# Optimization experiments

Measured on AMD Instinct MI355X. Metric: run time of the kernel, lower is better.

Reference implementation:

```python
import jax, jax.numpy as jnp
import numpy as np

N_HEAD = 4
N_FEAT = 256
D_K = N_FEAT // N_HEAD


def setup_inputs() -> dict:
    key = jax.random.key(0)
    ks = jax.random.split(key, 7)
    B, T, F = 8, 2048, N_FEAT
    return {
        "query": jax.random.normal(ks[0], (B, T, F), dtype=jnp.float32),
        "key": jax.random.normal(ks[1], (B, T, F), dtype=jnp.float32),
        "value": jax.random.normal(ks[2], (B, T, F), dtype=jnp.float32),
        "mask": jax.random.randint(ks[3], (B, 1, T), 0, 2, dtype=jnp.int32),
        "W_qkv": jax.random.normal(ks[4], (3 * F, 3 * F), dtype=jnp.float32) * 0.02,
        "b_qkv": jnp.zeros((3 * F,), dtype=jnp.float32),
        "W_out": jax.random.normal(ks[5], (F, F), dtype=jnp.float32) * 0.02,
        "b_out": jnp.zeros((F,), dtype=jnp.float32),
    }


def reference(query, key, value, mask, W_qkv, b_qkv, W_out, b_out):
    B, T, F = query.shape
    H, dk = N_HEAD, D_K
    # fused QKV projection on concatenated [q; k; v]  -> (B, T, 3F)
    qkv = jnp.concatenate([query, key, value], axis=-1) @ W_qkv.T + b_qkv
    qkv = qkv.reshape(B, T, H, 3 * dk)
    q, k, v = jnp.split(qkv, 3, axis=-1)          # each (B, T, H, dk)
    q = q.transpose(0, 2, 1, 3)                    # (B, H, T, dk)
    k = k.transpose(0, 2, 1, 3)
    v = v.transpose(0, 2, 1, 3)
    scores = jnp.einsum("bhqd,bhkd->bhqk", q, k) / jnp.sqrt(jnp.float32(dk))
    # mask: (B, 1, T) -> broadcast (B, 1, 1, T); positions where mask==0 are masked
    m = (mask[:, None, :, :] == 0)
    min_val = jnp.finfo(scores.dtype).min
    scores = jnp.where(m, min_val, scores)
    attn = jax.nn.softmax(scores, axis=-1)
    attn = jnp.where(m, jnp.float32(0.0), attn)    # zero masked probs, as in torch code
    x = jnp.einsum("bhqk,bhkd->bhqd", attn, v)     # (B, H, T, dk)
    x = x.transpose(0, 2, 1, 3).reshape(B, T, H * dk)
    return x @ W_out.T + b_out
```

## Files before the change

### kernel.cpp

```cpp
#include <hip/hip_runtime.h>
#include <hip/hip_bf16.h>

#define NB 8
#define NT 2048
#define NH 4
#define NF 256
#define NTF 768
#define NM (NB * NT)

typedef unsigned short u16;
typedef unsigned int u32;
typedef unsigned long long u64;
typedef u16 u16x8 __attribute__((ext_vector_type(8)));
typedef __bf16 bf16x8 __attribute__((ext_vector_type(8)));
typedef float f32x4 __attribute__((ext_vector_type(4)));
typedef float f32x16 __attribute__((ext_vector_type(16)));

__device__ __forceinline__ u16 bf16_rne(float f) {
    union { float f; unsigned u; } x; x.f = f;
    unsigned u = x.u;
    return (u16)((u + 0x7fffu + ((u >> 16) & 1u)) >> 16);
}

__device__ __forceinline__ int swz(int row, int colB) {
    return row * 128 + (colB ^ ((row & 7) << 4));
}

__device__ __forceinline__ void glds16(const void* g, void* l) {
    __builtin_amdgcn_global_load_lds(
        (const __attribute__((address_space(1))) void*)g,
        (__attribute__((address_space(3))) void*)l, 16, 0, 0);
}

__device__ __forceinline__ u32 pkbf16(float lo, float hi) {
    union { __bf16 h2[2]; u32 u; } t;
    t.h2[0] = (__bf16)lo; t.h2[1] = (__bf16)hi;
    return t.u;
}

__device__ __forceinline__ void pl32swap(u32& a, u32& b) {
    asm("v_permlane32_swap_b32 %0, %1" : "+v"(a), "+v"(b));
}

#define mfma16(A, B, C) __builtin_amdgcn_mfma_f32_16x16x32_bf16((A), (B), (C), 0, 0, 0)
#define mfma32(A, B, C) __builtin_amdgcn_mfma_f32_32x32x16_bf16((A), (B), (C), 0, 0, 0)

__global__ __launch_bounds__(256) void convert_all_kernel(
        const float* __restrict__ q, const float* __restrict__ k,
        const float* __restrict__ v, const float* __restrict__ wqkv,
        const float* __restrict__ wout, const int* __restrict__ mask,
        u16* __restrict__ xcat, u16* __restrict__ wqkvb,
        u16* __restrict__ woutb, float* __restrict__ maskadd) {
    int bid = blockIdx.x;
    if (bid < 6144) {
        int tid = bid * 256 + threadIdx.x;
        int row = tid / 96;
        int c8  = (tid % 96) * 8;
        const float* src; int c;
        if (c8 < NF)            { src = q; c = c8; }
        else if (c8 < 2 * NF)   { src = k; c = c8 - NF; }
        else                    { src = v; c = c8 - 2 * NF; }
        const float4* p = reinterpret_cast<const float4*>(src + (size_t)row * NF + c);
        float4 a = p[0], b = p[1];
        u16x8 o;
        o[0] = bf16_rne(a.x); o[1] = bf16_rne(a.y); o[2] = bf16_rne(a.z); o[3] = bf16_rne(a.w);
        o[4] = bf16_rne(b.x); o[5] = bf16_rne(b.y); o[6] = bf16_rne(b.z); o[7] = bf16_rne(b.w);
        *reinterpret_cast<u16x8*>(xcat + (size_t)row * NTF + c8) = o;
    } else if (bid < 6464) {
        int tid = (bid - 6144) * 256 + threadIdx.x;
        int i8 = tid * 8;
        const float* src; u16* dst; int off;
        if (i8 < NTF * NTF) { src = wqkv; dst = wqkvb; off = i8; }
        else                { src = wout; dst = woutb; off = i8 - NTF * NTF; }
        const float4* p = reinterpret_cast<const float4*>(src + off);
        float4 a = p[0], b = p[1];
        u16x8 o;
        o[0] = bf16_rne(a.x); o[1] = bf16_rne(a.y); o[2] = bf16_rne(a.z); o[3] = bf16_rne(a.w);
        o[4] = bf16_rne(b.x); o[5] = bf16_rne(b.y); o[6] = bf16_rne(b.z); o[7] = bf16_rne(b.w);
        *reinterpret_cast<u16x8*>(dst + off) = o;
    } else {
        int i = (bid - 6464) * 2048 + threadIdx.x * 8;
        int4 m0 = *reinterpret_cast<const int4*>(mask + i);
        int4 m1 = *reinterpret_cast<const int4*>(mask + i + 4);
        float4 f0 = { m0.x ? 0.f : -1e30f, m0.y ? 0.f : -1e30f,
                      m0.z ? 0.f : -1e30f, m0.w ? 0.f : -1e30f };
        float4 f1 = { m1.x ? 0.f : -1e30f, m1.y ? 0.f : -1e30f,
                      m1.z ? 0.f : -1e30f, m1.w ? 0.f : -1e30f };
        *reinterpret_cast<float4*>(maskadd + i) = f0;
        *reinterpret_cast<float4*>(maskadd + i + 4) = f1;
    }
}

__global__ __launch_bounds__(256) void gemm128_qkv_kernel(
        const u16* __restrict__ A, const u16* __restrict__ Bw,
        const float* __restrict__ bias, u16* __restrict__ QKV,
        u16* __restrict__ Vt) {
    __shared__ alignas(16) char smem[65536];
    char* As = smem;
    char* Bs = smem + 32768;
    constexpr int K = NTF;
    int m0 = blockIdx.x * 128, n0 = blockIdx.y * 128;
    int tid = threadIdx.x;
    int w = tid >> 6, lane = tid & 63, l15 = lane & 15, hi = lane >> 4;
    int wr = w >> 1, wc = w & 1;
    int r0 = tid >> 3, cb0 = (tid & 7) * 16;
    int gcb = cb0 ^ ((r0 & 7) << 4);
    int wo = w * 1024;

    const char* Ac = (const char*)A;
    const char* Bc = (const char*)Bw;
    const char* gA = Ac + (size_t)(m0 + r0) * (K * 2) + gcb;
    const char* gB = Bc + (size_t)(n0 + r0) * (K * 2) + gcb;
    const size_t rstep = (size_t)32 * (K * 2);

#pragma unroll
    for (int p = 0; p < 4; ++p) {
        glds16(gA + p * rstep, As + p * 4096 + wo);
        glds16(gB + p * rstep, Bs + p * 4096 + wo);
    }

    f32x4 acc[4][4];
#pragma unroll
    for (int fi = 0; fi < 4; ++fi)
#pragma unroll
        for (int fj = 0; fj < 4; ++fj) acc[fi][fj] = (f32x4){0.f, 0.f, 0.f, 0.f};

    constexpr int NKT = K / 64;
    for (int kt = 0; kt < NKT; ++kt) {
        int cur = kt & 1;
        __syncthreads();
        if (kt + 1 < NKT) {
            int off = (kt + 1) * 128;
            char* Ad = As + (cur ^ 1) * 16384;
            char* Bd = Bs + (cur ^ 1) * 16384;
#pragma unroll
            for (int p = 0; p < 4; ++p) {
                glds16(gA + p * rstep + off, Ad + p * 4096 + wo);
                glds16(gB + p * rstep + off, Bd + p * 4096 + wo);
            }
        }
        const char* Ax = As + cur * 16384;
        const char* Bx = Bs + cur * 16384;
#pragma unroll
        for (int ks = 0; ks < 2; ++ks) {
            bf16x8 af[4], bf[4];
#pragma unroll
            for (int fi = 0; fi < 4; ++fi)
                af[fi] = *reinterpret_cast<const bf16x8*>(
                    Ax + swz(wr * 64 + fi * 16 + l15, hi * 16 + ks * 64));
#pragma unroll
            for (int fj = 0; fj < 4; ++fj)
                bf[fj] = *reinterpret_cast<const bf16x8*>(
                    Bx + swz(wc * 64 + fj * 16 + l15, hi * 16 + ks * 64));
#pragma unroll
            for (int fi = 0; fi < 4; ++fi)
#pragma unroll
                for (int fj = 0; fj < 4; ++fj)
                    acc[fi][fj] = mfma16(af[fi], bf[fj], acc[fi][fj]);
        }
    }

    int g64 = (n0 >> 6) + wc;
    int typ = g64 % 3, h = g64 / 3;
    int rowBase = m0 + wr * 64;
    if (typ == 2) {
        int b = rowBase >> 11;
        int bh = b * NH + h;
#pragma unroll
        for (int fi = 0; fi < 4; ++fi) {
            int t = (rowBase + fi * 16 + hi * 4) & (NT - 1);
#pragma unroll
            for (int fj = 0; fj < 4; ++fj) {
                int d = fj * 16 + l15;
                float bv = bias[n0 + wc * 64 + d];
                u32 lo = pkbf16(acc[fi][fj][0] + bv, acc[fi][fj][1] + bv);
                u32 hi2 = pkbf16(acc[fi][fj][2] + bv, acc[fi][fj][3] + bv);
                u64 pk = (u64)lo | ((u64)hi2 << 32);
                *reinterpret_cast<u64*>(Vt + (size_t)(bh * 64 + d) * NT + t) = pk;
            }
        }
    } else {
#pragma unroll
        for (int fi = 0; fi < 4; ++fi) {
            int orow = rowBase + fi * 16 + hi * 4;
#pragma unroll
            for (int fj = 0; fj < 4; ++fj) {
                int col = n0 + wc * 64 + fj * 16 + l15;
                float bv = bias[col];
#pragma unroll
                for (int r = 0; r < 4; ++r)
                    QKV[(size_t)(orow + r) * NTF + col] = bf16_rne(acc[fi][fj][r] + bv);
            }
        }
    }
}

template<int N, int K>
__global__ __launch_bounds__(256) void gemm_kernel(
        const u16* __restrict__ A, const u16* __restrict__ Bw,
        const float* __restrict__ bias, float* __restrict__ Cout) {
    __shared__ alignas(16) char smem[32768];
    char* As = smem;
    char* Bs = smem + 16384;
    int m0 = blockIdx.x * 64, n0 = blockIdx.y * 64;
    int tid = threadIdx.x;
    int w = tid >> 6, lane = tid & 63, l15 = lane & 15, hi = lane >> 4;
    int r0 = tid >> 3, cb0 = (tid & 7) * 16;
    int gcb = cb0 ^ ((r0 & 7) << 4);
    int wo = w * 1024;

    const char* Ac = (const char*)A;
    const char* Bc = (const char*)Bw;
    const char* ga0 = Ac + (size_t)(m0 + r0) * (K * 2) + gcb;
    const char* ga1 = ga0 + (size_t)32 * (K * 2);
    const char* gb0 = Bc + (size_t)(n0 + r0) * (K * 2) + gcb;
    const char* gb1 = gb0 + (size_t)32 * (K * 2);

    glds16(ga0, As + wo); glds16(ga1, As + 4096 + wo);
    glds16(gb0, Bs + wo); glds16(gb1, Bs + 4096 + wo);

    f32x4 acc[4];
#pragma unroll
    for (int ct = 0; ct < 4; ++ct) acc[ct] = (f32x4){0.f, 0.f, 0.f, 0.f};

    constexpr int NKT = K / 64;
    for (int kt = 0; kt < NKT; ++kt) {
        int cur = kt & 1;
        __syncthreads();
        if (kt + 1 < NKT) {
            int off = (kt + 1) * 128;
            char* Ad = As + (cur ^ 1) * 8192;
            char* Bd = Bs + (cur ^ 1) * 8192;
            glds16(ga0 + off, Ad + wo); glds16(ga1 + off, Ad + 4096 + wo);
            glds16(gb0 + off, Bd + wo); glds16(gb1 + off, Bd + 4096 + wo);
        }
        const char* Ax = As + cur * 8192;
        const char* Bx = Bs + cur * 8192;
#pragma unroll
        for (int ks = 0; ks < 2; ++ks) {
            bf16x8 af = *reinterpret_cast<const bf16x8*>(Ax + swz(w * 16 + l15, hi * 16 + ks * 64));
#pragma unroll
            for (int ct = 0; ct < 4; ++ct) {
                bf16x8 bf = *reinterpret_cast<const bf16x8*>(Bx + swz(ct * 16 + l15, hi * 16 + ks * 64));
                acc[ct] = mfma16(af, bf, acc[ct]);
            }
        }
    }

    int orow = m0 + w * 16 + hi * 4;
#pragma unroll
    for (int ct = 0; ct < 4; ++ct) {
        int col = n0 + ct * 16 + l15;
        float bv = bias[col];
#pragma unroll
        for (int r = 0; r < 4; ++r)
            Cout[(size_t)(orow + r) * N + col] = acc[ct][r] + bv;
    }
}

__global__ __launch_bounds__(512, 4) void attn_kernel(
        const u16* __restrict__ qkv, const u16* __restrict__ vt,
        const float* __restrict__ maskadd, u16* __restrict__ xout) {
    int bh = blockIdx.x;
    int q0 = blockIdx.y * 128;
    int b = bh >> 2, h = bh & 3;
    __shared__ alignas(16) char smem[65536];
    int tid = threadIdx.x;
    int w = tid >> 6, lane = tid & 63;
    int l31 = lane & 31, hv = lane >> 5;
    int wq = w & 3, g = w >> 2;
    int r0 = tid >> 3, cb0 = (tid & 7) * 16;
    int gcb = cb0 ^ ((r0 & 7) << 4);
    int wo = w * 1024;
    const float SCALE = 0.125f * 1.44269504088896340736f;

    const char* qkvC = (const char*)qkv;
    const char* vtC  = (const char*)vt;
    const char* gk0 = qkvC + (size_t)(b * NT + r0) * 1536 + h * 384 + 128 + gcb;
    const char* gv0 = vtC + (size_t)(bh * 64 + r0) * (NT * 2) + gcb;

    glds16(gk0,         smem + wo);
    glds16(gk0 + 98304, smem + 8192 + wo);
    glds16(gv0,         smem + 32768 + wo);
    glds16(gv0 + 128,   smem + 32768 + 8192 + wo);

    const char* qrow = qkvC + (size_t)(b * NT + q0 + wq * 32 + l31) * 1536
                       + h * 384 + hv * 16;
    bf16x8 bQ0 = *reinterpret_cast<const bf16x8*>(qrow);
    bf16x8 bQ1 = *reinterpret_cast<const bf16x8*>(qrow + 32);
    bf16x8 bQ2 = *reinterpret_cast<const bf16x8*>(qrow + 64);
    bf16x8 bQ3 = *reinterpret_cast<const bf16x8*>(qrow + 96);

    f32x16 accO0 = 0.f, accO1 = 0.f;
    float ssum = 0.f;
    const float* gm = maskadd + (size_t)b * NT;

    for (int j = 0; j < 16; ++j) {
        int cur = j & 1;
        __syncthreads();
        if (j < 15) {
            int tn = 2 * (j + 1);
            char* Kd = smem + (cur ^ 1) * 16384;
            char* Vd = smem + 32768 + (cur ^ 1) * 16384;
            glds16(gk0 + (size_t)tn * 98304, Kd + wo);
            glds16(gk0 + (size_t)(tn + 1) * 98304, Kd + 8192 + wo);
            glds16(gv0 + (size_t)tn * 128, Vd + wo);
            glds16(gv0 + (size_t)(tn + 1) * 128, Vd + 8192 + wo);
        }
        int t = 2 * j + g;
        const char* Kx = smem + g * 8192 + cur * 16384;
        const char* Vx = smem + 32768 + g * 8192 + cur * 16384;

        f32x16 s0 = 0.f, s1 = 0.f;
        __builtin_amdgcn_s_setprio(1);
#pragma unroll
        for (int ks = 0; ks < 4; ++ks) {
            bf16x8 a0 = *reinterpret_cast<const bf16x8*>(Kx + swz(l31, ks * 32 + hv * 16));
            bf16x8 a1 = *reinterpret_cast<const bf16x8*>(Kx + swz(32 + l31, ks * 32 + hv * 16));
            bf16x8 bq = (ks == 0) ? bQ0 : (ks == 1) ? bQ1 : (ks == 2) ? bQ2 : bQ3;
            s0 = mfma32(a0, bq, s0);
            s1 = mfma32(a1, bq, s1);
        }
        __builtin_amdgcn_s_setprio(0);

        const float* mt = gm + t * 64;
#pragma unroll
        for (int rq = 0; rq < 4; ++rq) {
            f32x4 md0 = *reinterpret_cast<const f32x4*>(mt + rq * 8 + 4 * hv);
            f32x4 md1 = *reinterpret_cast<const f32x4*>(mt + 32 + rq * 8 + 4 * hv);
#pragma unroll
            for (int e = 0; e < 4; ++e) {
                s0[rq * 4 + e] = __builtin_amdgcn_exp2f(
                    __builtin_fmaf(s0[rq * 4 + e], SCALE, md0[e]));
                s1[rq * 4 + e] = __builtin_amdgcn_exp2f(
                    __builtin_fmaf(s1[rq * 4 + e], SCALE, md1[e]));
            }
        }
        {
            f32x16 rv = s0 + s1;
            union { f32x16 v; f32x4 q[4]; } u; u.v = rv;
            f32x4 r4 = (u.q[0] + u.q[1]) + (u.q[2] + u.q[3]);
            ssum += (r4[0] + r4[1]) + (r4[2] + r4[3]);
        }

        u32 pka0[4], pkb0[4], pka1[4], pkb1[4];
#pragma unroll
        for (int rq = 0; rq < 4; ++rq) {
            pka0[rq] = pkbf16(s0[rq * 4 + 0], s0[rq * 4 + 1]);
            pkb0[rq] = pkbf16(s0[rq * 4 + 2], s0[rq * 4 + 3]);
            pka1[rq] = pkbf16(s1[rq * 4 + 0], s1[rq * 4 + 1]);
            pkb1[rq] = pkbf16(s1[rq * 4 + 2], s1[rq * 4 + 3]);
        }
        __builtin_amdgcn_s_setprio(1);
#pragma unroll
        for (int s4 = 0; s4 < 4; ++s4) {
            const int kb = s4 >> 1, sp = (s4 & 1) * 2;
            u32 B0, B1, B2, B3;
            if (kb == 0) { B0 = pka0[sp]; B2 = pka0[sp + 1]; B1 = pkb0[sp]; B3 = pkb0[sp + 1]; }
            else         { B0 = pka1[sp]; B2 = pka1[sp + 1]; B1 = pkb1[sp]; B3 = pkb1[sp + 1]; }
            pl32swap(B0, B2);
            pl32swap(B1, B3);
            union { u32 u4[4]; bf16x8 v; } bp;
            bp.u4[0] = B0; bp.u4[1] = B1; bp.u4[2] = B2; bp.u4[3] = B3;
            bf16x8 av0 = *reinterpret_cast<const bf16x8*>(Vx + swz(l31, s4 * 32 + hv * 16));
            bf16x8 av1 = *reinterpret_cast<const bf16x8*>(Vx + swz(32 + l31, s4 * 32 + hv * 16));
            accO0 = mfma32(av0, bp.v, accO0);
            accO1 = mfma32(av1, bp.v, accO1);
        }
        __builtin_amdgcn_s_setprio(0);
    }

    ssum += __shfl_xor(ssum, 32, 64);
    __syncthreads();
    float* sS = reinterpret_cast<float*>(smem + 32768);
    if (g == 1) {
        union { f32x16 v; f32x4 q[4]; } o0, o1; o0.v = accO0; o1.v = accO1;
#pragma unroll
        for (int i = 0; i < 4; ++i) {
            *reinterpret_cast<f32x4*>(smem + wq * 8192 + i * 1024 + lane * 16) = o0.q[i];
            *reinterpret_cast<f32x4*>(smem + wq * 8192 + (4 + i) * 1024 + lane * 16) = o1.q[i];
        }
        if (lane < 32) sS[wq * 32 + l31] = ssum;
    }
    __syncthreads();
    if (g == 0) {
        union { f32x16 v; f32x4 q[4]; } o0, o1; o0.v = accO0; o1.v = accO1;
#pragma unroll
        for (int i = 0; i < 4; ++i) {
            o0.q[i] += *reinterpret_cast<const f32x4*>(smem + wq * 8192 + i * 1024 + lane * 16);
            o1.q[i] += *reinterpret_cast<const f32x4*>(smem + wq * 8192 + (4 + i) * 1024 + lane * 16);
        }
        float stot = ssum + sS[wq * 32 + l31];
        float inv = stot > 0.f ? 1.0f / stot : 0.0f;
        int qg = b * NT + q0 + wq * 32 + l31;
#pragma unroll
        for (int db = 0; db < 2; ++db) {
            const float* of = db ? (const float*)&o1.v : (const float*)&o0.v;
#pragma unroll
            for (int rq = 0; rq < 4; ++rq) {
                u32 lo = pkbf16(of[rq * 4 + 0] * inv, of[rq * 4 + 1] * inv);
                u32 hi2 = pkbf16(of[rq * 4 + 2] * inv, of[rq * 4 + 3] * inv);
                u64 pk = (u64)lo | ((u64)hi2 << 32);
                int d = db * 32 + rq * 8 + 4 * hv;
                *reinterpret_cast<u64*>(xout + (size_t)qg * NF + h * 64 + d) = pk;
            }
        }
    }
}

extern "C" void kernel_launch(void* const* d_in, const int* in_sizes, int n_in,
                              void* d_out, int out_size, void* d_ws, size_t ws_size,
                              hipStream_t stream) {
    const float* q    = (const float*)d_in[0];
    const float* k    = (const float*)d_in[1];
    const float* v    = (const float*)d_in[2];
    const int*   mask = (const int*)d_in[3];
    const float* wqkv = (const float*)d_in[4];
    const float* bqkv = (const float*)d_in[5];
    const float* wout = (const float*)d_in[6];
    const float* bout = (const float*)d_in[7];
    float* out = (float*)d_out;

    char* ws = (char*)d_ws;
    u16*   Xcat    = (u16*)(ws);
    u16*   QKV     = (u16*)(ws + 25165824);
    u16*   Vt      = (u16*)(ws + 50331648);
    u16*   Xattn   = (u16*)(ws + 58720256);
    u16*   Wqkvb   = (u16*)(ws + 67108864);
    u16*   Woutb   = (u16*)(ws + 68288512);
    float* Maskadd = (float*)(ws + 68419584);

    convert_all_kernel<<<6472, 256, 0, stream>>>(q, k, v, wqkv, wout, mask,
                                                 Xcat, Wqkvb, Woutb, Maskadd);
    gemm128_qkv_kernel<<<dim3(NM / 128, NTF / 128), 256, 0, stream>>>(
        Xcat, Wqkvb, bqkv, QKV, Vt);
    attn_kernel<<<dim3(NB * NH, NT / 128), 512, 0, stream>>>(QKV, Vt, Maskadd, Xattn);
    gemm_kernel<NF, NF><<<dim3(NM / 64, NF / 64), 256, 0, stream>>>(
        Xattn, Woutb, bout, out);
}
```

Before: 101.2 us.

## Fuse fp32-to-bf16 activation conversion into QKV GEMM A-tile loading

Removes the separate conversion of query/key/value into a concatenated bf16 buffer. The QKV GEMM now loads fp32 activations directly into registers, converts them to bf16 and stores them into swizzled shared memory, with the load overlapped with the MFMA loop. This avoids writing and re-reading a 24 MB intermediate and one large kernel launch. In exchange, each A tile is read in fp32 by every column block and converted redundantly, which raises register use (launch bounds set to 2 blocks per CU).

After: 104.2 us. 3.0% more time.

```diff
diff --git a/kernel.cpp b/kernel.cpp
--- a/kernel.cpp
+++ b/kernel.cpp
@@ -12,6 +12,7 @@
 typedef unsigned int u32;
 typedef unsigned long long u64;
 typedef u16 u16x8 __attribute__((ext_vector_type(8)));
+typedef u32 u32x4 __attribute__((ext_vector_type(4)));
 typedef __bf16 bf16x8 __attribute__((ext_vector_type(8)));
 typedef float f32x4 __attribute__((ext_vector_type(4)));
 typedef float f32x16 __attribute__((ext_vector_type(16)));
@@ -45,29 +46,13 @@
 #define mfma16(A, B, C) __builtin_amdgcn_mfma_f32_16x16x32_bf16((A), (B), (C), 0, 0, 0)
 #define mfma32(A, B, C) __builtin_amdgcn_mfma_f32_32x32x16_bf16((A), (B), (C), 0, 0, 0)
 
-__global__ __launch_bounds__(256) void convert_all_kernel(
-        const float* __restrict__ q, const float* __restrict__ k,
-        const float* __restrict__ v, const float* __restrict__ wqkv,
-        const float* __restrict__ wout, const int* __restrict__ mask,
-        u16* __restrict__ xcat, u16* __restrict__ wqkvb,
+__global__ __launch_bounds__(256) void convert_wm_kernel(
+        const float* __restrict__ wqkv, const float* __restrict__ wout,
+        const int* __restrict__ mask, u16* __restrict__ wqkvb,
         u16* __restrict__ woutb, float* __restrict__ maskadd) {
     int bid = blockIdx.x;
-    if (bid < 6144) {
+    if (bid < 320) {
         int tid = bid * 256 + threadIdx.x;
-        int row = tid / 96;
-        int c8  = (tid % 96) * 8;
-        const float* src; int c;
-        if (c8 < NF)            { src = q; c = c8; }
-        else if (c8 < 2 * NF)   { src = k; c = c8 - NF; }
-        else                    { src = v; c = c8 - 2 * NF; }
-        const float4* p = reinterpret_cast<const float4*>(src + (size_t)row * NF + c);
-        float4 a = p[0], b = p[1];
-        u16x8 o;
-        o[0] = bf16_rne(a.x); o[1] = bf16_rne(a.y); o[2] = bf16_rne(a.z); o[3] = bf16_rne(a.w);
-        o[4] = bf16_rne(b.x); o[5] = bf16_rne(b.y); o[6] = bf16_rne(b.z); o[7] = bf16_rne(b.w);
-        *reinterpret_cast<u16x8*>(xcat + (size_t)row * NTF + c8) = o;
-    } else if (bid < 6464) {
-        int tid = (bid - 6144) * 256 + threadIdx.x;
         int i8 = tid * 8;
         const float* src; u16* dst; int off;
         if (i8 < NTF * NTF) { src = wqkv; dst = wqkvb; off = i8; }
@@ -79,7 +64,7 @@
         o[4] = bf16_rne(b.x); o[5] = bf16_rne(b.y); o[6] = bf16_rne(b.z); o[7] = bf16_rne(b.w);
         *reinterpret_cast<u16x8*>(dst + off) = o;
     } else {
-        int i = (bid - 6464) * 2048 + threadIdx.x * 8;
+        int i = (bid - 320) * 2048 + threadIdx.x * 8;
         int4 m0 = *reinterpret_cast<const int4*>(mask + i);
         int4 m1 = *reinterpret_cast<const int4*>(mask + i + 4);
         float4 f0 = { m0.x ? 0.f : -1e30f, m0.y ? 0.f : -1e30f,
@@ -91,8 +76,9 @@
     }
 }
 
-__global__ __launch_bounds__(256) void gemm128_qkv_kernel(
-        const u16* __restrict__ A, const u16* __restrict__ Bw,
+__global__ __launch_bounds__(256, 2) void gemm128_qkv_kernel(
+        const float* __restrict__ Xq, const float* __restrict__ Xk,
+        const float* __restrict__ Xv, const u16* __restrict__ Bw,
         const float* __restrict__ bias, u16* __restrict__ QKV,
         u16* __restrict__ Vt) {
     __shared__ alignas(16) char smem[65536];
@@ -103,21 +89,42 @@
     int tid = threadIdx.x;
     int w = tid >> 6, lane = tid & 63, l15 = lane & 15, hi = lane >> 4;
     int wr = w >> 1, wc = w & 1;
-    int r0 = tid >> 3, cb0 = (tid & 7) * 16;
+    int r0 = tid >> 3, c8 = (tid & 7) * 8;
+    int cb0 = (tid & 7) * 16;
     int gcb = cb0 ^ ((r0 & 7) << 4);
     int wo = w * 1024;
 
-    const char* Ac = (const char*)A;
     const char* Bc = (const char*)Bw;
-    const char* gA = Ac + (size_t)(m0 + r0) * (K * 2) + gcb;
     const char* gB = Bc + (size_t)(n0 + r0) * (K * 2) + gcb;
     const size_t rstep = (size_t)32 * (K * 2);
 
-#pragma unroll
-    for (int p = 0; p < 4; ++p) {
-        glds16(gA + p * rstep, As + p * 4096 + wo);
-        glds16(gB + p * rstep, Bs + p * 4096 + wo);
-    }
+    float4 a_reg[4][2];
+    auto a_load = [&](int kt) {
+        const float* src = (kt < 4) ? Xq : (kt < 8) ? Xk : Xv;
+        int colbase = (kt & 3) * 64;
+#pragma unroll
+        for (int p = 0; p < 4; ++p) {
+            const float* sp = src + (size_t)(m0 + r0 + p * 32) * NF + colbase + c8;
+            a_reg[p][0] = *reinterpret_cast<const float4*>(sp);
+            a_reg[p][1] = *reinterpret_cast<const float4*>(sp + 4);
+        }
+    };
+    auto a_store = [&](char* Ad) {
+#pragma unroll
+        for (int p = 0; p < 4; ++p) {
+            u32x4 pk;
+            pk[0] = pkbf16(a_reg[p][0].x, a_reg[p][0].y);
+            pk[1] = pkbf16(a_reg[p][0].z, a_reg[p][0].w);
+            pk[2] = pkbf16(a_reg[p][1].x, a_reg[p][1].y);
+            pk[3] = pkbf16(a_reg[p][1].z, a_reg[p][1].w);
+            *reinterpret_cast<u32x4*>(Ad + swz(r0 + p * 32, c8 * 2)) = pk;
+        }
+    };
+
+    a_load(0);
+#pragma unroll
+    for (int p = 0; p < 4; ++p) glds16(gB + p * rstep, Bs + p * 4096 + wo);
+    a_store(As);
 
     f32x4 acc[4][4];
 #pragma unroll
@@ -131,13 +138,10 @@
         __syncthreads();
         if (kt + 1 < NKT) {
             int off = (kt + 1) * 128;
-            char* Ad = As + (cur ^ 1) * 16384;
             char* Bd = Bs + (cur ^ 1) * 16384;
-#pragma unroll
-            for (int p = 0; p < 4; ++p) {
-                glds16(gA + p * rstep + off, Ad + p * 4096 + wo);
-                glds16(gB + p * rstep + off, Bd + p * 4096 + wo);
-            }
+            a_load(kt + 1);
+#pragma unroll
+            for (int p = 0; p < 4; ++p) glds16(gB + p * rstep + off, Bd + p * 4096 + wo);
         }
         const char* Ax = As + cur * 16384;
         const char* Bx = Bs + cur * 16384;
@@ -158,6 +162,7 @@
                 for (int fj = 0; fj < 4; ++fj)
                     acc[fi][fj] = mfma16(af[fi], bf[fj], acc[fi][fj]);
         }
+        if (kt + 1 < NKT) a_store(As + (cur ^ 1) * 16384);
     }
 
     int g64 = (n0 >> 6) + wc;
@@ -422,18 +427,16 @@
     float* out = (float*)d_out;
 
     char* ws = (char*)d_ws;
-    u16*   Xcat    = (u16*)(ws);
-    u16*   QKV     = (u16*)(ws + 25165824);
-    u16*   Vt      = (u16*)(ws + 50331648);
-    u16*   Xattn   = (u16*)(ws + 58720256);
-    u16*   Wqkvb   = (u16*)(ws + 67108864);
-    u16*   Woutb   = (u16*)(ws + 68288512);
-    float* Maskadd = (float*)(ws + 68419584);
-
-    convert_all_kernel<<<6472, 256, 0, stream>>>(q, k, v, wqkv, wout, mask,
-                                                 Xcat, Wqkvb, Woutb, Maskadd);
+    u16*   QKV     = (u16*)(ws);
+    u16*   Vt      = (u16*)(ws + 25165824);
+    u16*   Xattn   = (u16*)(ws + 33554432);
+    u16*   Wqkvb   = (u16*)(ws + 41943040);
+    u16*   Woutb   = (u16*)(ws + 43122688);
+    float* Maskadd = (float*)(ws + 43253760);
+
+    convert_wm_kernel<<<328, 256, 0, stream>>>(wqkv, wout, mask, Wqkvb, Woutb, Maskadd);
     gemm128_qkv_kernel<<<dim3(NM / 128, NTF / 128), 256, 0, stream>>>(
-        Xcat, Wqkvb, bqkv, QKV, Vt);
+        q, k, v, Wqkvb, bqkv, QKV, Vt);
     attn_kernel<<<dim3(NB * NH, NT / 128), 512, 0, stream>>>(QKV, Vt, Maskadd, Xattn);
     gemm_kernel<NF, NF><<<dim3(NM / 64, NF / 64), 256, 0, stream>>>(
         Xattn, Woutb, bout, out);
```

## Drop key-split in attention and reuse 128x128 GEMM template for output projection

Applied to the files above, without the earlier changes.

The attention kernel goes from 512 threads, where two wave groups split the key range and combine partial outputs through shared memory, to 256 threads where each wave walks every key tile for 32 query rows. Shared memory per block halves and the cross-group reduction and its extra syncs are removed. The output projection switches from a 64x64 tile GEMM to a templated version of the 128x128 QKV GEMM with an fp32 output mode. The attention change trades intra-block parallelism for less LDS use and no reduction step, so it relies on more resident blocks to hide latency. The larger output GEMM tiles reduce the block count to 512.

Result: slower. 110.8 us (+9.5%).

```diff
diff --git a/kernel.cpp b/kernel.cpp
--- a/kernel.cpp
+++ b/kernel.cpp
@@ -91,14 +91,14 @@
     }
 }
 
-__global__ __launch_bounds__(256) void gemm128_qkv_kernel(
+template<int N, int K, int MODE>
+__global__ __launch_bounds__(256) void gemm128_kernel(
         const u16* __restrict__ A, const u16* __restrict__ Bw,
-        const float* __restrict__ bias, u16* __restrict__ QKV,
+        const float* __restrict__ bias, void* __restrict__ Cout,
         u16* __restrict__ Vt) {
     __shared__ alignas(16) char smem[65536];
     char* As = smem;
     char* Bs = smem + 32768;
-    constexpr int K = NTF;
     int m0 = blockIdx.x * 128, n0 = blockIdx.y * 128;
     int tid = threadIdx.x;
     int w = tid >> 6, lane = tid & 63, l15 = lane & 15, hi = lane >> 4;
@@ -160,23 +160,39 @@
         }
     }
 
-    int g64 = (n0 >> 6) + wc;
-    int typ = g64 % 3, h = g64 / 3;
     int rowBase = m0 + wr * 64;
-    if (typ == 2) {
-        int b = rowBase >> 11;
-        int bh = b * NH + h;
-#pragma unroll
-        for (int fi = 0; fi < 4; ++fi) {
-            int t = (rowBase + fi * 16 + hi * 4) & (NT - 1);
-#pragma unroll
-            for (int fj = 0; fj < 4; ++fj) {
-                int d = fj * 16 + l15;
-                float bv = bias[n0 + wc * 64 + d];
-                u32 lo = pkbf16(acc[fi][fj][0] + bv, acc[fi][fj][1] + bv);
-                u32 hi2 = pkbf16(acc[fi][fj][2] + bv, acc[fi][fj][3] + bv);
-                u64 pk = (u64)lo | ((u64)hi2 << 32);
-                *reinterpret_cast<u64*>(Vt + (size_t)(bh * 64 + d) * NT + t) = pk;
+    if constexpr (MODE == 2) {
+        int g64 = (n0 >> 6) + wc;
+        int typ = g64 % 3, h = g64 / 3;
+        if (typ == 2) {
+            int b = rowBase >> 11;
+            int bh = b * NH + h;
+#pragma unroll
+            for (int fi = 0; fi < 4; ++fi) {
+                int t = (rowBase + fi * 16 + hi * 4) & (NT - 1);
+#pragma unroll
+                for (int fj = 0; fj < 4; ++fj) {
+                    int d = fj * 16 + l15;
+                    float bv = bias[n0 + wc * 64 + d];
+                    u32 lo = pkbf16(acc[fi][fj][0] + bv, acc[fi][fj][1] + bv);
+                    u32 hi2 = pkbf16(acc[fi][fj][2] + bv, acc[fi][fj][3] + bv);
+                    u64 pk = (u64)lo | ((u64)hi2 << 32);
+                    *reinterpret_cast<u64*>(Vt + (size_t)(bh * 64 + d) * NT + t) = pk;
+                }
+            }
+        } else {
+#pragma unroll
+            for (int fi = 0; fi < 4; ++fi) {
+                int orow = rowBase + fi * 16 + hi * 4;
+#pragma unroll
+                for (int fj = 0; fj < 4; ++fj) {
+                    int col = n0 + wc * 64 + fj * 16 + l15;
+                    float bv = bias[col];
+#pragma unroll
+                    for (int r = 0; r < 4; ++r)
+                        reinterpret_cast<u16*>(Cout)[(size_t)(orow + r) * N + col] =
+                            bf16_rne(acc[fi][fj][r] + bv);
+                }
             }
         }
     } else {
@@ -189,86 +205,23 @@
                 float bv = bias[col];
 #pragma unroll
                 for (int r = 0; r < 4; ++r)
-                    QKV[(size_t)(orow + r) * NTF + col] = bf16_rne(acc[fi][fj][r] + bv);
-            }
-        }
-    }
-}
-
-template<int N, int K>
-__global__ __launch_bounds__(256) void gemm_kernel(
-        const u16* __restrict__ A, const u16* __restrict__ Bw,
-        const float* __restrict__ bias, float* __restrict__ Cout) {
-    __shared__ alignas(16) char smem[32768];
-    char* As = smem;
-    char* Bs = smem + 16384;
-    int m0 = blockIdx.x * 64, n0 = blockIdx.y * 64;
-    int tid = threadIdx.x;
-    int w = tid >> 6, lane = tid & 63, l15 = lane & 15, hi = lane >> 4;
-    int r0 = tid >> 3, cb0 = (tid & 7) * 16;
-    int gcb = cb0 ^ ((r0 & 7) << 4);
-    int wo = w * 1024;
-
-    const char* Ac = (const char*)A;
-    const char* Bc = (const char*)Bw;
-    const char* ga0 = Ac + (size_t)(m0 + r0) * (K * 2) + gcb;
-    const char* ga1 = ga0 + (size_t)32 * (K * 2);
-    const char* gb0 = Bc + (size_t)(n0 + r0) * (K * 2) + gcb;
-    const char* gb1 = gb0 + (size_t)32 * (K * 2);
-
-    glds16(ga0, As + wo); glds16(ga1, As + 4096 + wo);
-    glds16(gb0, Bs + wo); glds16(gb1, Bs + 4096 + wo);
-
-    f32x4 acc[4];
-#pragma unroll
-    for (int ct = 0; ct < 4; ++ct) acc[ct] = (f32x4){0.f, 0.f, 0.f, 0.f};
-
-    constexpr int NKT = K / 64;
-    for (int kt = 0; kt < NKT; ++kt) {
-        int cur = kt & 1;
-        __syncthreads();
-        if (kt + 1 < NKT) {
-            int off = (kt + 1) * 128;
-            char* Ad = As + (cur ^ 1) * 8192;
-            char* Bd = Bs + (cur ^ 1) * 8192;
-            glds16(ga0 + off, Ad + wo); glds16(ga1 + off, Ad + 4096 + wo);
-            glds16(gb0 + off, Bd + wo); glds16(gb1 + off, Bd + 4096 + wo);
-        }
-        const char* Ax = As + cur * 8192;
-        const char* Bx = Bs + cur * 8192;
-#pragma unroll
-        for (int ks = 0; ks < 2; ++ks) {
-            bf16x8 af = *reinterpret_cast<const bf16x8*>(Ax + swz(w * 16 + l15, hi * 16 + ks * 64));
-#pragma unroll
-            for (int ct = 0; ct < 4; ++ct) {
-                bf16x8 bf = *reinterpret_cast<const bf16x8*>(Bx + swz(ct * 16 + l15, hi * 16 + ks * 64));
-                acc[ct] = mfma16(af, bf, acc[ct]);
-            }
-        }
-    }
-
-    int orow = m0 + w * 16 + hi * 4;
-#pragma unroll
-    for (int ct = 0; ct < 4; ++ct) {
-        int col = n0 + ct * 16 + l15;
-        float bv = bias[col];
-#pragma unroll
-        for (int r = 0; r < 4; ++r)
-            Cout[(size_t)(orow + r) * N + col] = acc[ct][r] + bv;
-    }
-}
-
-__global__ __launch_bounds__(512, 4) void attn_kernel(
+                    reinterpret_cast<float*>(Cout)[(size_t)(orow + r) * N + col] =
+                        acc[fi][fj][r] + bv;
+            }
+        }
+    }
+}
+
+__global__ __launch_bounds__(256, 4) void attn_kernel(
         const u16* __restrict__ qkv, const u16* __restrict__ vt,
         const float* __restrict__ maskadd, u16* __restrict__ xout) {
     int bh = blockIdx.x;
     int q0 = blockIdx.y * 128;
     int b = bh >> 2, h = bh & 3;
-    __shared__ alignas(16) char smem[65536];
+    __shared__ alignas(16) char smem[32768];
     int tid = threadIdx.x;
     int w = tid >> 6, lane = tid & 63;
     int l31 = lane & 31, hv = lane >> 5;
-    int wq = w & 3, g = w >> 2;
     int r0 = tid >> 3, cb0 = (tid & 7) * 16;
     int gcb = cb0 ^ ((r0 & 7) << 4);
     int wo = w * 1024;
@@ -278,13 +231,14 @@
     const char* vtC  = (const char*)vt;
     const char* gk0 = qkvC + (size_t)(b * NT + r0) * 1536 + h * 384 + 128 + gcb;
     const char* gv0 = vtC + (size_t)(bh * 64 + r0) * (NT * 2) + gcb;
-
-    glds16(gk0,         smem + wo);
-    glds16(gk0 + 98304, smem + 8192 + wo);
-    glds16(gv0,         smem + 32768 + wo);
-    glds16(gv0 + 128,   smem + 32768 + 8192 + wo);
-
-    const char* qrow = qkvC + (size_t)(b * NT + q0 + wq * 32 + l31) * 1536
+    const float* gm = maskadd + (size_t)b * NT;
+
+    glds16(gk0,              smem + wo);
+    glds16(gk0 + 32 * 1536,  smem + 4096 + wo);
+    glds16(gv0,              smem + 16384 + wo);
+    glds16(gv0 + 32 * 4096,  smem + 16384 + 4096 + wo);
+
+    const char* qrow = qkvC + (size_t)(b * NT + q0 + w * 32 + l31) * 1536
                        + h * 384 + hv * 16;
     bf16x8 bQ0 = *reinterpret_cast<const bf16x8*>(qrow);
     bf16x8 bQ1 = *reinterpret_cast<const bf16x8*>(qrow + 32);
@@ -293,117 +247,91 @@
 
     f32x16 accO0 = 0.f, accO1 = 0.f;
     float ssum = 0.f;
-    const float* gm = maskadd + (size_t)b * NT;
-
-    for (int j = 0; j < 16; ++j) {
+
+    for (int j = 0; j < NT / 64; ++j) {
         int cur = j & 1;
         __syncthreads();
-        if (j < 15) {
-            int tn = 2 * (j + 1);
-            char* Kd = smem + (cur ^ 1) * 16384;
-            char* Vd = smem + 32768 + (cur ^ 1) * 16384;
-            glds16(gk0 + (size_t)tn * 98304, Kd + wo);
-            glds16(gk0 + (size_t)(tn + 1) * 98304, Kd + 8192 + wo);
-            glds16(gv0 + (size_t)tn * 128, Vd + wo);
-            glds16(gv0 + (size_t)(tn + 1) * 128, Vd + 8192 + wo);
-        }
-        int t = 2 * j + g;
-        const char* Kx = smem + g * 8192 + cur * 16384;
-        const char* Vx = smem + 32768 + g * 8192 + cur * 16384;
-
-        f32x16 s0 = 0.f, s1 = 0.f;
-        __builtin_amdgcn_s_setprio(1);
-#pragma unroll
-        for (int ks = 0; ks < 4; ++ks) {
-            bf16x8 a0 = *reinterpret_cast<const bf16x8*>(Kx + swz(l31, ks * 32 + hv * 16));
-            bf16x8 a1 = *reinterpret_cast<const bf16x8*>(Kx + swz(32 + l31, ks * 32 + hv * 16));
-            bf16x8 bq = (ks == 0) ? bQ0 : (ks == 1) ? bQ1 : (ks == 2) ? bQ2 : bQ3;
-            s0 = mfma32(a0, bq, s0);
-            s1 = mfma32(a1, bq, s1);
-        }
-        __builtin_amdgcn_s_setprio(0);
-
-        const float* mt = gm + t * 64;
+        if (j < NT / 64 - 1) {
+            char* Kd = smem + (cur ^ 1) * 8192;
+            char* Vd = smem + 16384 + (cur ^ 1) * 8192;
+            size_t ko = (size_t)(j + 1) * 98304;
+            size_t vo2 = (size_t)(j + 1) * 128;
+            glds16(gk0 + ko,             Kd + wo);
+            glds16(gk0 + ko + 32 * 1536, Kd + 4096 + wo);
+            glds16(gv0 + vo2,            Vd + wo);
+            glds16(gv0 + vo2 + 32 * 4096, Vd + 4096 + wo);
+        }
+        const char* Kx = smem + cur * 8192;
+        const char* Vx = smem + 16384 + cur * 8192;
+        const float* mt = gm + j * 64;
+
+#pragma unroll
+        for (int kb = 0; kb < 2; ++kb) {
+            f32x16 s = 0.f;
+            __builtin_amdgcn_s_setprio(1);
+#pragma unroll
+            for (int ks = 0; ks < 4; ++ks) {
+                bf16x8 a = *reinterpret_cast<const bf16x8*>(
+                    Kx + swz(kb * 32 + l31, ks * 32 + hv * 16));
+                bf16x8 bq = (ks == 0) ? bQ0 : (ks == 1) ? bQ1 : (ks == 2) ? bQ2 : bQ3;
+                s = mfma32(a, bq, s);
+            }
+            __builtin_amdgcn_s_setprio(0);
+
+#pragma unroll
+            for (int rq = 0; rq < 4; ++rq) {
+                f32x4 md = *reinterpret_cast<const f32x4*>(mt + kb * 32 + rq * 8 + 4 * hv);
+#pragma unroll
+                for (int e = 0; e < 4; ++e)
+                    s[rq * 4 + e] = __builtin_amdgcn_exp2f(
+                        __builtin_fmaf(s[rq * 4 + e], SCALE, md[e]));
+            }
+            {
+                union { f32x16 v; f32x4 q[4]; } u; u.v = s;
+                f32x4 r4 = (u.q[0] + u.q[1]) + (u.q[2] + u.q[3]);
+                ssum += (r4[0] + r4[1]) + (r4[2] + r4[3]);
+            }
+            u32 pa[4], pb[4];
+#pragma unroll
+            for (int rq = 0; rq < 4; ++rq) {
+                pa[rq] = pkbf16(s[rq * 4 + 0], s[rq * 4 + 1]);
+                pb[rq] = pkbf16(s[rq * 4 + 2], s[rq * 4 + 3]);
+            }
+            __builtin_amdgcn_s_setprio(1);
+#pragma unroll
+            for (int sp2 = 0; sp2 < 2; ++sp2) {
+                const int sp = sp2 * 2;
+                u32 B0 = pa[sp], B2 = pa[sp + 1], B1 = pb[sp], B3 = pb[sp + 1];
+                pl32swap(B0, B2);
+                pl32swap(B1, B3);
+                union { u32 u4[4]; bf16x8 v; } bp;
+                bp.u4[0] = B0; bp.u4[1] = B1; bp.u4[2] = B2; bp.u4[3] = B3;
+                int s4 = 2 * kb + sp2;
+                bf16x8 av0 = *reinterpret_cast<const bf16x8*>(
+                    Vx + swz(l31, s4 * 32 + hv * 16));
+                bf16x8 av1 = *reinterpret_cast<const bf16x8*>(
+                    Vx + swz(32 + l31, s4 * 32 + hv * 16));
+                accO0 = mfma32(av0, bp.v, accO0);
+                accO1 = mfma32(av1, bp.v, accO1);
+            }
+            __builtin_amdgcn_s_setprio(0);
+        }
+    }
+
+    ssum += __shfl_xor(ssum, 32, 64);
+    float inv = ssum > 0.f ? 1.0f / ssum : 0.0f;
+    int qg = b * NT + q0 + w * 32 + l31;
+    union { f32x16 v; float f[16]; } o0, o1; o0.v = accO0; o1.v = accO1;
+#pragma unroll
+    for (int db = 0; db < 2; ++db) {
+        const float* of = db ? o1.f : o0.f;
 #pragma unroll
         for (int rq = 0; rq < 4; ++rq) {
-            f32x4 md0 = *reinterpret_cast<const f32x4*>(mt + rq * 8 + 4 * hv);
-            f32x4 md1 = *reinterpret_cast<const f32x4*>(mt + 32 + rq * 8 + 4 * hv);
-#pragma unroll
-            for (int e = 0; e < 4; ++e) {
-                s0[rq * 4 + e] = __builtin_amdgcn_exp2f(
-                    __builtin_fmaf(s0[rq * 4 + e], SCALE, md0[e]));
-                s1[rq * 4 + e] = __builtin_amdgcn_exp2f(
-                    __builtin_fmaf(s1[rq * 4 + e], SCALE, md1[e]));
-            }
-        }
-        {
-            f32x16 rv = s0 + s1;
-            union { f32x16 v; f32x4 q[4]; } u; u.v = rv;
-            f32x4 r4 = (u.q[0] + u.q[1]) + (u.q[2] + u.q[3]);
-            ssum += (r4[0] + r4[1]) + (r4[2] + r4[3]);
-        }
-
-        u32 pka0[4], pkb0[4], pka1[4], pkb1[4];
-#pragma unroll
-        for (int rq = 0; rq < 4; ++rq) {
-            pka0[rq] = pkbf16(s0[rq * 4 + 0], s0[rq * 4 + 1]);
-            pkb0[rq] = pkbf16(s0[rq * 4 + 2], s0[rq * 4 + 3]);
-            pka1[rq] = pkbf16(s1[rq * 4 + 0], s1[rq * 4 + 1]);
-            pkb1[rq] = pkbf16(s1[rq * 4 + 2], s1[rq * 4 + 3]);
-        }
-        __builtin_amdgcn_s_setprio(1);
-#pragma unroll
-        for (int s4 = 0; s4 < 4; ++s4) {
-            const int kb = s4 >> 1, sp = (s4 & 1) * 2;
-            u32 B0, B1, B2, B3;
-            if (kb == 0) { B0 = pka0[sp]; B2 = pka0[sp + 1]; B1 = pkb0[sp]; B3 = pkb0[sp + 1]; }
-            else         { B0 = pka1[sp]; B2 = pka1[sp + 1]; B1 = pkb1[sp]; B3 = pkb1[sp + 1]; }
-            pl32swap(B0, B2);
-            pl32swap(B1, B3);
-            union { u32 u4[4]; bf16x8 v; } bp;
-            bp.u4[0] = B0; bp.u4[1] = B1; bp.u4[2] = B2; bp.u4[3] = B3;
-            bf16x8 av0 = *reinterpret_cast<const bf16x8*>(Vx + swz(l31, s4 * 32 + hv * 16));
-            bf16x8 av1 = *reinterpret_cast<const bf16x8*>(Vx + swz(32 + l31, s4 * 32 + hv * 16));
-            accO0 = mfma32(av0, bp.v, accO0);
-            accO1 = mfma32(av1, bp.v, accO1);
-        }
-        __builtin_amdgcn_s_setprio(0);
-    }
-
-    ssum += __shfl_xor(ssum, 32, 64);
-    __syncthreads();
-    float* sS = reinterpret_cast<float*>(smem + 32768);
-    if (g == 1) {
-        union { f32x16 v; f32x4 q[4]; } o0, o1; o0.v = accO0; o1.v = accO1;
-#pragma unroll
-        for (int i = 0; i < 4; ++i) {
-            *reinterpret_cast<f32x4*>(smem + wq * 8192 + i * 1024 + lane * 16) = o0.q[i];
-            *reinterpret_cast<f32x4*>(smem + wq * 8192 + (4 + i) * 1024 + lane * 16) = o1.q[i];
-        }
-        if (lane < 32) sS[wq * 32 + l31] = ssum;
-    }
-    __syncthreads();
-    if (g == 0) {
-        union { f32x16 v; f32x4 q[4]; } o0, o1; o0.v = accO0; o1.v = accO1;
-#pragma unroll
-        for (int i = 0; i < 4; ++i) {
-            o0.q[i] += *reinterpret_cast<const f32x4*>(smem + wq * 8192 + i * 1024 + lane * 16);
-            o1.q[i] += *reinterpret_cast<const f32x4*>(smem + wq * 8192 + (4 + i) * 1024 + lane * 16);
-        }
-        float stot = ssum + sS[wq * 32 + l31];
-        float inv = stot > 0.f ? 1.0f / stot : 0.0f;
-        int qg = b * NT + q0 + wq * 32 + l31;
-#pragma unroll
-        for (int db = 0; db < 2; ++db) {
-            const float* of = db ? (const float*)&o1.v : (const float*)&o0.v;
-#pragma unroll
-            for (int rq = 0; rq < 4; ++rq) {
-                u32 lo = pkbf16(of[rq * 4 + 0] * inv, of[rq * 4 + 1] * inv);
-                u32 hi2 = pkbf16(of[rq * 4 + 2] * inv, of[rq * 4 + 3] * inv);
-                u64 pk = (u64)lo | ((u64)hi2 << 32);
-                int d = db * 32 + rq * 8 + 4 * hv;
-                *reinterpret_cast<u64*>(xout + (size_t)qg * NF + h * 64 + d) = pk;
-            }
+            u32 lo = pkbf16(of[rq * 4 + 0] * inv, of[rq * 4 + 1] * inv);
+            u32 hi2 = pkbf16(of[rq * 4 + 2] * inv, of[rq * 4 + 3] * inv);
+            u64 pk = (u64)lo | ((u64)hi2 << 32);
+            int d = db * 32 + rq * 8 + 4 * hv;
+            *reinterpret_cast<u64*>(xout + (size_t)qg * NF + h * 64 + d) = pk;
         }
     }
 }
@@ -432,9 +360,9 @@
 
     convert_all_kernel<<<6472, 256, 0, stream>>>(q, k, v, wqkv, wout, mask,
                                                  Xcat, Wqkvb, Woutb, Maskadd);
-    gemm128_qkv_kernel<<<dim3(NM / 128, NTF / 128), 256, 0, stream>>>(
+    gemm128_kernel<NTF, NTF, 2><<<dim3(NM / 128, NTF / 128), 256, 0, stream>>>(
         Xcat, Wqkvb, bqkv, QKV, Vt);
-    attn_kernel<<<dim3(NB * NH, NT / 128), 512, 0, stream>>>(QKV, Vt, Maskadd, Xattn);
-    gemm_kernel<NF, NF><<<dim3(NM / 64, NF / 64), 256, 0, stream>>>(
-        Xattn, Woutb, bout, out);
-}
+    attn_kernel<<<dim3(NB * NH, NT / 128), 256, 0, stream>>>(QKV, Vt, Maskadd, Xattn);
+    gemm128_kernel<NF, NF, 1><<<dim3(NM / 128, NF / 128), 256, 0, stream>>>(
+        Xattn, Woutb, bout, out, nullptr);
+}
```

## Use 128x128 tiled GEMM for output projection and hoist mask loads in attention

Applied to the files above, without the earlier changes.

The 64x64 output-projection GEMM is replaced by a templated version of the 128x128 QKV GEMM, writing fp32 output, so each tile reuses more data. In the attention loop, the additive-mask loads are moved ahead of the K/V prefetch and QK MFMAs, fenced by sched barriers, so their global latency overlaps the matrix math. The trade-offs are that the out-projection grid shrinks to 512 blocks, which may underfill the GPU, and that holding the mask values longer raises register pressure.

New measurement: 122.5 us. +21.1%, slower.

```diff
diff --git a/kernel.cpp b/kernel.cpp
--- a/kernel.cpp
+++ b/kernel.cpp
@@ -91,14 +91,14 @@
     }
 }
 
-__global__ __launch_bounds__(256) void gemm128_qkv_kernel(
+template<int N, int K, int MODE>
+__global__ __launch_bounds__(256) void gemm128_kernel(
         const u16* __restrict__ A, const u16* __restrict__ Bw,
-        const float* __restrict__ bias, u16* __restrict__ QKV,
+        const float* __restrict__ bias, void* __restrict__ Cout,
         u16* __restrict__ Vt) {
     __shared__ alignas(16) char smem[65536];
     char* As = smem;
     char* Bs = smem + 32768;
-    constexpr int K = NTF;
     int m0 = blockIdx.x * 128, n0 = blockIdx.y * 128;
     int tid = threadIdx.x;
     int w = tid >> 6, lane = tid & 63, l15 = lane & 15, hi = lane >> 4;
@@ -160,23 +160,39 @@
         }
     }
 
-    int g64 = (n0 >> 6) + wc;
-    int typ = g64 % 3, h = g64 / 3;
     int rowBase = m0 + wr * 64;
-    if (typ == 2) {
-        int b = rowBase >> 11;
-        int bh = b * NH + h;
-#pragma unroll
-        for (int fi = 0; fi < 4; ++fi) {
-            int t = (rowBase + fi * 16 + hi * 4) & (NT - 1);
-#pragma unroll
-            for (int fj = 0; fj < 4; ++fj) {
-                int d = fj * 16 + l15;
-                float bv = bias[n0 + wc * 64 + d];
-                u32 lo = pkbf16(acc[fi][fj][0] + bv, acc[fi][fj][1] + bv);
-                u32 hi2 = pkbf16(acc[fi][fj][2] + bv, acc[fi][fj][3] + bv);
-                u64 pk = (u64)lo | ((u64)hi2 << 32);
-                *reinterpret_cast<u64*>(Vt + (size_t)(bh * 64 + d) * NT + t) = pk;
+    if constexpr (MODE == 2) {
+        int g64 = (n0 >> 6) + wc;
+        int typ = g64 % 3, h = g64 / 3;
+        if (typ == 2) {
+            int b = rowBase >> 11;
+            int bh = b * NH + h;
+#pragma unroll
+            for (int fi = 0; fi < 4; ++fi) {
+                int t = (rowBase + fi * 16 + hi * 4) & (NT - 1);
+#pragma unroll
+                for (int fj = 0; fj < 4; ++fj) {
+                    int d = fj * 16 + l15;
+                    float bv = bias[n0 + wc * 64 + d];
+                    u32 lo = pkbf16(acc[fi][fj][0] + bv, acc[fi][fj][1] + bv);
+                    u32 hi2 = pkbf16(acc[fi][fj][2] + bv, acc[fi][fj][3] + bv);
+                    u64 pk = (u64)lo | ((u64)hi2 << 32);
+                    *reinterpret_cast<u64*>(Vt + (size_t)(bh * 64 + d) * NT + t) = pk;
+                }
+            }
+        } else {
+#pragma unroll
+            for (int fi = 0; fi < 4; ++fi) {
+                int orow = rowBase + fi * 16 + hi * 4;
+#pragma unroll
+                for (int fj = 0; fj < 4; ++fj) {
+                    int col = n0 + wc * 64 + fj * 16 + l15;
+                    float bv = bias[col];
+#pragma unroll
+                    for (int r = 0; r < 4; ++r)
+                        reinterpret_cast<u16*>(Cout)[(size_t)(orow + r) * N + col] =
+                            bf16_rne(acc[fi][fj][r] + bv);
+                }
             }
         }
     } else {
@@ -189,72 +205,10 @@
                 float bv = bias[col];
 #pragma unroll
                 for (int r = 0; r < 4; ++r)
-                    QKV[(size_t)(orow + r) * NTF + col] = bf16_rne(acc[fi][fj][r] + bv);
-            }
-        }
-    }
-}
-
-template<int N, int K>
-__global__ __launch_bounds__(256) void gemm_kernel(
-        const u16* __restrict__ A, const u16* __restrict__ Bw,
-        const float* __restrict__ bias, float* __restrict__ Cout) {
-    __shared__ alignas(16) char smem[32768];
-    char* As = smem;
-    char* Bs = smem + 16384;
-    int m0 = blockIdx.x * 64, n0 = blockIdx.y * 64;
-    int tid = threadIdx.x;
-    int w = tid >> 6, lane = tid & 63, l15 = lane & 15, hi = lane >> 4;
-    int r0 = tid >> 3, cb0 = (tid & 7) * 16;
-    int gcb = cb0 ^ ((r0 & 7) << 4);
-    int wo = w * 1024;
-
-    const char* Ac = (const char*)A;
-    const char* Bc = (const char*)Bw;
-    const char* ga0 = Ac + (size_t)(m0 + r0) * (K * 2) + gcb;
-    const char* ga1 = ga0 + (size_t)32 * (K * 2);
-    const char* gb0 = Bc + (size_t)(n0 + r0) * (K * 2) + gcb;
-    const char* gb1 = gb0 + (size_t)32 * (K * 2);
-
-    glds16(ga0, As + wo); glds16(ga1, As + 4096 + wo);
-    glds16(gb0, Bs + wo); glds16(gb1, Bs + 4096 + wo);
-
-    f32x4 acc[4];
-#pragma unroll
-    for (int ct = 0; ct < 4; ++ct) acc[ct] = (f32x4){0.f, 0.f, 0.f, 0.f};
-
-    constexpr int NKT = K / 64;
-    for (int kt = 0; kt < NKT; ++kt) {
-        int cur = kt & 1;
-        __syncthreads();
-        if (kt + 1 < NKT) {
-            int off = (kt + 1) * 128;
-            char* Ad = As + (cur ^ 1) * 8192;
-            char* Bd = Bs + (cur ^ 1) * 8192;
-            glds16(ga0 + off, Ad + wo); glds16(ga1 + off, Ad + 4096 + wo);
-            glds16(gb0 + off, Bd + wo); glds16(gb1 + off, Bd + 4096 + wo);
-        }
-        const char* Ax = As + cur * 8192;
-        const char* Bx = Bs + cur * 8192;
-#pragma unroll
-        for (int ks = 0; ks < 2; ++ks) {
-            bf16x8 af = *reinterpret_cast<const bf16x8*>(Ax + swz(w * 16 + l15, hi * 16 + ks * 64));
-#pragma unroll
-            for (int ct = 0; ct < 4; ++ct) {
-                bf16x8 bf = *reinterpret_cast<const bf16x8*>(Bx + swz(ct * 16 + l15, hi * 16 + ks * 64));
-                acc[ct] = mfma16(af, bf, acc[ct]);
-            }
-        }
-    }
-
-    int orow = m0 + w * 16 + hi * 4;
-#pragma unroll
-    for (int ct = 0; ct < 4; ++ct) {
-        int col = n0 + ct * 16 + l15;
-        float bv = bias[col];
-#pragma unroll
-        for (int r = 0; r < 4; ++r)
-            Cout[(size_t)(orow + r) * N + col] = acc[ct][r] + bv;
+                    reinterpret_cast<float*>(Cout)[(size_t)(orow + r) * N + col] =
+                        acc[fi][fj][r] + bv;
+            }
+        }
     }
 }
 
@@ -278,6 +232,7 @@
     const char* vtC  = (const char*)vt;
     const char* gk0 = qkvC + (size_t)(b * NT + r0) * 1536 + h * 384 + 128 + gcb;
     const char* gv0 = vtC + (size_t)(bh * 64 + r0) * (NT * 2) + gcb;
+    const float* gm = maskadd + (size_t)b * NT;
 
     glds16(gk0,         smem + wo);
     glds16(gk0 + 98304, smem + 8192 + wo);
@@ -293,11 +248,20 @@
 
     f32x16 accO0 = 0.f, accO1 = 0.f;
     float ssum = 0.f;
-    const float* gm = maskadd + (size_t)b * NT;
 
     for (int j = 0; j < 16; ++j) {
         int cur = j & 1;
         __syncthreads();
+        __builtin_amdgcn_sched_barrier(0);
+        int t = 2 * j + g;
+        const float* mt = gm + t * 64;
+        f32x4 md0[4], md1[4];
+#pragma unroll
+        for (int rq = 0; rq < 4; ++rq) {
+            md0[rq] = *reinterpret_cast<const f32x4*>(mt + rq * 8 + 4 * hv);
+            md1[rq] = *reinterpret_cast<const f32x4*>(mt + 32 + rq * 8 + 4 * hv);
+        }
+        __builtin_amdgcn_sched_barrier(0);
         if (j < 15) {
             int tn = 2 * (j + 1);
             char* Kd = smem + (cur ^ 1) * 16384;
@@ -307,7 +271,6 @@
             glds16(gv0 + (size_t)tn * 128, Vd + wo);
             glds16(gv0 + (size_t)(tn + 1) * 128, Vd + 8192 + wo);
         }
-        int t = 2 * j + g;
         const char* Kx = smem + g * 8192 + cur * 16384;
         const char* Vx = smem + 32768 + g * 8192 + cur * 16384;
 
@@ -323,17 +286,14 @@
         }
         __builtin_amdgcn_s_setprio(0);
 
-        const float* mt = gm + t * 64;
 #pragma unroll
         for (int rq = 0; rq < 4; ++rq) {
-            f32x4 md0 = *reinterpret_cast<const f32x4*>(mt + rq * 8 + 4 * hv);
-            f32x4 md1 = *reinterpret_cast<const f32x4*>(mt + 32 + rq * 8 + 4 * hv);
 #pragma unroll
             for (int e = 0; e < 4; ++e) {
                 s0[rq * 4 + e] = __builtin_amdgcn_exp2f(
-                    __builtin_fmaf(s0[rq * 4 + e], SCALE, md0[e]));
+                    __builtin_fmaf(s0[rq * 4 + e], SCALE, md0[rq][e]));
                 s1[rq * 4 + e] = __builtin_amdgcn_exp2f(
-                    __builtin_fmaf(s1[rq * 4 + e], SCALE, md1[e]));
+                    __builtin_fmaf(s1[rq * 4 + e], SCALE, md1[rq][e]));
             }
         }
         {
@@ -432,9 +392,9 @@
 
     convert_all_kernel<<<6472, 256, 0, stream>>>(q, k, v, wqkv, wout, mask,
                                                  Xcat, Wqkvb, Woutb, Maskadd);
-    gemm128_qkv_kernel<<<dim3(NM / 128, NTF / 128), 256, 0, stream>>>(
+    gemm128_kernel<NTF, NTF, 2><<<dim3(NM / 128, NTF / 128), 256, 0, stream>>>(
         Xcat, Wqkvb, bqkv, QKV, Vt);
     attn_kernel<<<dim3(NB * NH, NT / 128), 512, 0, stream>>>(QKV, Vt, Maskadd, Xattn);
-    gemm_kernel<NF, NF><<<dim3(NM / 64, NF / 64), 256, 0, stream>>>(
-        Xattn, Woutb, bout, out);
-}
+    gemm128_kernel<NF, NF, 1><<<dim3(NM / 128, NF / 128), 256, 0, stream>>>(
+        Xattn, Woutb, bout, out, nullptr);
+}
```
